# Performance work log

Hardware: AMD Instinct MI355X
Metric: run time of the kernel (lower is better)

The kernel has to match this reference:

```python
import jax, jax.numpy as jnp
import numpy as np

N_NODES = 100000
N_EDGES = 1600000
D_FEAT = 64
D_OUT = 64


def setup_inputs() -> dict:
    key = jax.random.key(0)
    ks = jax.random.split(key, 8)
    return {
        "feat": jax.random.normal(ks[0], (N_NODES, D_FEAT), dtype=jnp.float32),
        "emb": jax.random.normal(ks[1], (N_NODES, D_OUT), dtype=jnp.float32),
        "W1": jax.random.normal(ks[2], (D_OUT, D_FEAT), dtype=jnp.float32) * 0.1,
        "b1": jax.random.normal(ks[3], (D_OUT,), dtype=jnp.float32) * 0.1,
        "W2": jax.random.normal(ks[4], (D_OUT, D_OUT), dtype=jnp.float32) * 0.1,
        "b2": jax.random.normal(ks[5], (D_OUT,), dtype=jnp.float32) * 0.1,
        "edge_src": jax.random.randint(ks[6], (N_EDGES,), 0, N_NODES, dtype=jnp.int32),
        "edge_dst": jax.random.randint(ks[7], (N_EDGES,), 0, N_NODES, dtype=jnp.int32),
    }


def reference(feat, emb, W1, b1, W2, b2, edge_src, edge_dst):
    # n2v: per-node neighbor embedding sum (vectorized gather + segment-sum)
    n_nodes = feat.shape[0]
    nbr_sum = jax.ops.segment_sum(emb[edge_src], edge_dst, num_segments=n_nodes)  # [N, D_OUT]
    new_emb = jax.nn.relu(feat @ W1.T + b1 + nbr_sum @ W2.T + b2)  # [N, D_OUT]
    # g2v: graph embedding = sum of node embeddings
    graph_emb = new_emb.sum(axis=0)  # [D_OUT]
    return graph_emb
```

## Files before the change

### kernel.cpp

```cpp
#include <hip/hip_runtime.h>

#define N_NODES 100000
#define N_EDGES 1600000
#define D 64
#define CAP 32
#define OVF_CAP 8192
#define N_TILES 1563
#define NR 8
#define SLICE_EDGES 2048
#define N_SLICES 782
#define R1_BLOCKS 64
#define R1_ROWS 25
#define ASTRIDE 136

#define NB2 782
#define BCAP2 2560
#define EPB 8192
#define P1_BLOCKS 196
#define CVT_BLOCKS 128

typedef int    vint4  __attribute__((ext_vector_type(4)));
typedef short  s16x4  __attribute__((ext_vector_type(4)));
typedef short  s16x8  __attribute__((ext_vector_type(8)));
typedef float  f32x2  __attribute__((ext_vector_type(2)));
typedef float  f32x4  __attribute__((ext_vector_type(4)));
typedef __bf16 bf16x8 __attribute__((ext_vector_type(8)));

__device__ inline short f2bf(float f) {
    unsigned u = __builtin_bit_cast(unsigned, f);
    u += 0x7fffu + ((u >> 16) & 1u);
    return (short)(u >> 16);
}
__device__ inline s16x4 f2bf4(float4 v) {
    s16x4 r; r.x = f2bf(v.x); r.y = f2bf(v.y); r.z = f2bf(v.z); r.w = f2bf(v.w);
    return r;
}
__device__ inline float bf2f(short s) {
    return __builtin_bit_cast(float, ((unsigned)(unsigned short)s) << 16);
}

#define WS_SLOTS_OFF  401408
#define WS_ACC_OFF    13201408
#define WS_ACC16_OFF  13201408
#define WS_FEAT16_OFF 26001408
#define WS_OVFC_OFF   38801408
#define WS_OVF_OFF    38801424
#define WS_PART_OFF   38867200
#define WS_PART2_OFF  39267328
#define WS_EMB8_OFF   39283712
#define WS_W16_OFF    45683712
#define WS_NEEDED     (WS_PART2_OFF + R1_BLOCKS * 64 * 4)
#define WS_NEEDED16   (WS_W16_OFF + 64 * 128 * 2)

__global__ __launch_bounds__(512) void part_kernel(
    const int* __restrict__ edge_src, const int* __restrict__ edge_dst,
    int* __restrict__ bcnt, int* __restrict__ bkt,
    int* __restrict__ ovf_cnt, int2* __restrict__ ovf,
    const float* __restrict__ emb, unsigned* __restrict__ emb8,
    const float* __restrict__ feat, short* __restrict__ feat16,
    const float* __restrict__ W1, const float* __restrict__ W2,
    short* __restrict__ w16) {
    const int tid = threadIdx.x;
    if (blockIdx.x >= P1_BLOCKS) {
        const int rid = blockIdx.x - P1_BLOCKS;
        {
            const float4* e4 = (const float4*)emb;
            for (unsigned j = rid * 512 + tid; j < (unsigned)(N_NODES * D / 4);
                 j += CVT_BLOCKS * 512) {
                float4 v = e4[j];
                int w = 0;
                w = __builtin_amdgcn_cvt_pk_fp8_f32(v.x, v.y, w, false);
                w = __builtin_amdgcn_cvt_pk_fp8_f32(v.z, v.w, w, true);
                emb8[j] = (unsigned)w;
            }
        }
        {
            const float4* f4 = (const float4*)feat;
            for (unsigned k = rid * 512 + tid; k < (unsigned)(N_NODES * D / 8);
                 k += CVT_BLOCKS * 512) {
                float4 a = f4[k * 2];
                float4 b = f4[k * 2 + 1];
                s16x4 lo = f2bf4(a), hi = f2bf4(b);
                s16x8 pk = {lo.x, lo.y, lo.z, lo.w, hi.x, hi.y, hi.z, hi.w};
                *(s16x8*)&feat16[k * 8] = pk;
            }
        }
        if (rid == 0) {
            const float4* W1v = (const float4*)W1;
            const float4* W2v = (const float4*)W2;
            for (int k = tid; k < 64 * 16; k += 512) {
                const int row = k >> 4, c = k & 15;
                const float4 a = (c < 8) ? W1v[row * 16 + c * 2]
                                         : W2v[row * 16 + (c - 8) * 2];
                const float4 b = (c < 8) ? W1v[row * 16 + c * 2 + 1]
                                         : W2v[row * 16 + (c - 8) * 2 + 1];
                s16x4 lo = f2bf4(a), hi = f2bf4(b);
                s16x8 pk = {lo.x, lo.y, lo.z, lo.w, hi.x, hi.y, hi.z, hi.w};
                *(s16x8*)&w16[row * 128 + c * 8] = pk;
            }
        }
        return;
    }

    __shared__ int stage[EPB];
    __shared__ unsigned short bid[EPB];
    __shared__ int scA[1024];
    __shared__ int scB[1024];
    __shared__ int hist[NB2];
    int* const cur   = scB;
    int* const gbase = scA;

    const int e0 = blockIdx.x * EPB;
    for (int i = tid; i < NB2; i += 512) hist[i] = 0;
    __syncthreads();

    int ss[16], dd[16];
#pragma unroll
    for (int i = 0; i < 16; ++i) {
        const int e = e0 + i * 512 + tid;
        if (e < N_EDGES) { ss[i] = edge_src[e]; dd[i] = edge_dst[e]; }
        else             { ss[i] = 0; dd[i] = -1; }
    }

#pragma unroll
    for (int i = 0; i < 16; ++i)
        if (dd[i] >= 0) atomicAdd(&hist[dd[i] >> 7], 1);
    __syncthreads();

    scA[tid]       = (tid < NB2) ? hist[tid] : 0;
    scA[tid + 512] = 0;
    if (tid + 512 < NB2) scA[tid + 512] = hist[tid + 512];
    __syncthreads();
    {
        int* sA = scA;
        int* sB = scB;
        for (int off = 1; off < 1024; off <<= 1) {
            const int i1 = tid + 512;
            const int v0 = sA[tid] + ((tid >= off) ? sA[tid - off] : 0);
            const int v1 = sA[i1] + sA[i1 - off];
            sB[tid] = v0; sB[i1] = v1;
            __syncthreads();
            int* t = sA; sA = sB; sB = t;
        }
    }
    const int tot = scA[NB2 - 1];
    for (int i = tid; i < NB2; i += 512) cur[i] = scA[i] - hist[i];
    __syncthreads();

#pragma unroll
    for (int i = 0; i < 16; ++i) {
        if (dd[i] >= 0) {
            const int b = dd[i] >> 7;
            const int pos = atomicAdd(&cur[b], 1);
            stage[pos] = (ss[i] << 7) | (dd[i] & 127);
            bid[pos] = (unsigned short)b;
        }
    }
    for (int i = tid; i < NB2; i += 512)
        gbase[i] = atomicAdd(&bcnt[i], hist[i]);
    __syncthreads();

    for (int j = tid; j < tot; j += 512) {
        const int pk = stage[j];
        const int b  = bid[j];
        const int gpos = gbase[b] + (j - (cur[b] - hist[b]));
        if (gpos < BCAP2) {
            bkt[b * BCAP2 + gpos] = pk;
        } else {
            int oj = atomicAdd(ovf_cnt, 1);
            if (oj < OVF_CAP) ovf[oj] = make_int2(pk >> 7, (b << 7) | (pk & 127));
        }
    }
}

__global__ __launch_bounds__(512) void fill2_kernel(
    const int* __restrict__ bcnt, const int* __restrict__ bkt,
    int* __restrict__ cnt, int* __restrict__ slots,
    int* __restrict__ ovf_cnt, int2* __restrict__ ovf) {
    __shared__ int lcnt[128];
    const int b = blockIdx.x;
    const int tid = threadIdx.x;
    if (tid < 128) lcnt[tid] = 0;
    __syncthreads();
    int n = bcnt[b];
    if (n > BCAP2) n = BCAP2;
    for (int i = tid; i < n; i += 512) {
        const int pk = bkt[b * BCAP2 + i];
        const int dl = pk & 127;
        const int pos = atomicAdd(&lcnt[dl], 1);
        const int v = (b << 7) | dl;
        if (pos < CAP) {
            slots[v * CAP + pos] = pk >> 7;
        } else {
            int j = atomicAdd(ovf_cnt, 1);
            if (j < OVF_CAP) ovf[j] = make_int2(pk >> 7, v);
        }
    }
    __syncthreads();
    if (tid < 128) {
        const int v = (b << 7) | tid;
        if (v < N_NODES) cnt[v] = lcnt[tid];
    }
}

__global__ __launch_bounds__(256) void gather8_kernel(
    const unsigned* __restrict__ emb8, const int* __restrict__ cnt,
    const int* __restrict__ slots, short* __restrict__ acc16) {
    const int lane = threadIdx.x & 63;
    const int wave = threadIdx.x >> 6;
    const int v = blockIdx.x * 4 + wave;
    const int q = lane >> 4;
    const int c = lane & 15;
    int deg = cnt[v];
    if (deg > CAP) deg = CAP;
    const int si = slots[v * CAP + (lane & (CAP - 1))];

    float4 sum = make_float4(0.f, 0.f, 0.f, 0.f);
    for (int e = 0; e < deg; e += 8) {
        const int i0 = e + q, i1 = e + 4 + q;
        const int s0 = __shfl(si, i0 & (CAP - 1));
        const int s1 = __shfl(si, i1 & (CAP - 1));
        unsigned x0 = 0u, x1 = 0u;
        if (i0 < deg) x0 = emb8[(unsigned)s0 * 16 + c];
        if (i1 < deg) x1 = emb8[(unsigned)s1 * 16 + c];
        const f32x2 a0 = __builtin_amdgcn_cvt_pk_f32_fp8((int)x0, false);
        const f32x2 a1 = __builtin_amdgcn_cvt_pk_f32_fp8((int)x0, true);
        const f32x2 b0 = __builtin_amdgcn_cvt_pk_f32_fp8((int)x1, false);
        const f32x2 b1 = __builtin_amdgcn_cvt_pk_f32_fp8((int)x1, true);
        sum.x += a0.x + b0.x;
        sum.y += a0.y + b0.y;
        sum.z += a1.x + b1.x;
        sum.w += a1.y + b1.y;
    }
#pragma unroll
    for (int off = 16; off < 64; off <<= 1) {
        sum.x += __shfl_xor(sum.x, off);
        sum.y += __shfl_xor(sum.y, off);
        sum.z += __shfl_xor(sum.z, off);
        sum.w += __shfl_xor(sum.w, off);
    }
    if (q == 0) {
        *(s16x4*)&acc16[v * D + c * 4] = f2bf4(sum);
    }
}

__global__ __launch_bounds__(64) void ovf2_kernel(
    const float* __restrict__ emb, const int* __restrict__ ovf_cnt,
    const int2* __restrict__ ovf, short* __restrict__ acc16) {
    int n = *ovf_cnt;
    if (n > OVF_CAP) n = OVF_CAP;
    const int l = threadIdx.x;
    for (int i = 0; i < n; ++i) {
        const int2 e = ovf[i];
        const float a = bf2f(acc16[e.y * D + l]) + emb[e.x * D + l];
        acc16[e.y * D + l] = f2bf(a);
    }
}

__global__ __launch_bounds__(256) void fill_kernel(
    const int* __restrict__ edge_src, const int* __restrict__ edge_dst,
    int* __restrict__ cnt, int* __restrict__ slots,
    int* __restrict__ ovf_cnt, int2* __restrict__ ovf) {
    const int r = blockIdx.x & (NR - 1);
    if (r == 7) return;
    const int slice = blockIdx.x >> 3;
    const int base_e = slice * SLICE_EDGES + threadIdx.x * 8;
    if (base_e >= N_EDGES) return;
    const vint4* s4 = (const vint4*)(edge_src + base_e);
    const vint4* d4 = (const vint4*)(edge_dst + base_e);
    vint4 a0 = __builtin_nontemporal_load(s4);
    vint4 a1 = __builtin_nontemporal_load(s4 + 1);
    vint4 b0 = __builtin_nontemporal_load(d4);
    vint4 b1 = __builtin_nontemporal_load(d4 + 1);
    int ss[8] = {a0.x, a0.y, a0.z, a0.w, a1.x, a1.y, a1.z, a1.w};
    int dd[8] = {b0.x, b0.y, b0.z, b0.w, b1.x, b1.y, b1.z, b1.w};
    int pos[8];
#pragma unroll
    for (int i = 0; i < 8; ++i) {
        pos[i] = ((dd[i] >> 14) == r) ? atomicAdd(&cnt[dd[i]], 1) : -1;
    }
#pragma unroll
    for (int i = 0; i < 8; ++i) {
        if (pos[i] >= 0 && pos[i] < CAP) slots[dd[i] * CAP + pos[i]] = ss[i];
    }
#pragma unroll
    for (int i = 0; i < 8; ++i) {
        if (pos[i] >= CAP) {
            int j = atomicAdd(ovf_cnt, 1);
            if (j < OVF_CAP) ovf[j] = make_int2(ss[i], dd[i]);
        }
    }
}

__global__ __launch_bounds__(256) void gather_kernel(
    const float* __restrict__ emb, const int* __restrict__ cnt,
    const int* __restrict__ slots, float* __restrict__ acc) {
    const int lane = threadIdx.x & 63;
    const int wave = threadIdx.x >> 6;
    const int v = blockIdx.x * 4 + wave;
    const int q  = lane >> 4;
    const int c4 = lane & 15;
    int deg = cnt[v];
    if (deg > CAP) deg = CAP;
    const int si = slots[v * CAP + (lane & (CAP - 1))];
    const float4* emb4 = (const float4*)emb;

    float4 sum = make_float4(0.f, 0.f, 0.f, 0.f);
    for (int e = 0; e < deg; e += 4) {
        const int idx = e + q;
        const int s = __shfl(si, idx & (CAP - 1));
        if (idx < deg) {
            float4 a = emb4[s * 16 + c4];
            sum.x += a.x; sum.y += a.y; sum.z += a.z; sum.w += a.w;
        }
    }
#pragma unroll
    for (int off = 16; off < 64; off <<= 1) {
        sum.x += __shfl_xor(sum.x, off);
        sum.y += __shfl_xor(sum.y, off);
        sum.z += __shfl_xor(sum.z, off);
        sum.w += __shfl_xor(sum.w, off);
    }
    if (q == 0) {
        ((float4*)acc)[v * 16 + c4] = sum;
    }
}

__global__ __launch_bounds__(256) void ovf_kernel(
    const float* __restrict__ emb, const int* __restrict__ ovf_cnt,
    const int2* __restrict__ ovf, float* __restrict__ acc) {
    int n = *ovf_cnt;
    if (n > OVF_CAP) n = OVF_CAP;
    const int lane = threadIdx.x & 63;
    const int wv = (blockIdx.x * 256 + threadIdx.x) >> 6;
    const int nwaves = (gridDim.x * 256) >> 6;
    for (int i = wv; i < n; i += nwaves) {
        int2 e = ovf[i];
        unsafeAtomicAdd(&acc[e.y * D + lane], emb[e.x * D + lane]);
    }
}

__global__ __launch_bounds__(256) void scatter_kernel(
    const float* __restrict__ emb,
    const int* __restrict__ edge_src, const int* __restrict__ edge_dst,
    float* __restrict__ acc) {
    int gid = blockIdx.x * 256 + threadIdx.x;
    int e = gid >> 6;
    int c = gid & 63;
    unsafeAtomicAdd(&acc[edge_dst[e] * D + c], emb[edge_src[e] * D + c]);
}

__global__ __launch_bounds__(256) void final16_kernel(
    const short* __restrict__ feat16, const short* __restrict__ acc16,
    const short* __restrict__ w16, const float* __restrict__ b1,
    const float* __restrict__ b2, float* __restrict__ partials) {
    __shared__ short A_s[64 * ASTRIDE];
    __shared__ short W_s[64 * ASTRIDE];
    __shared__ float red[4][64];

    const int tid  = threadIdx.x;
    const int lane = tid & 63;
    const int wave = tid >> 6;
    const int quad = lane >> 4;
    const int col  = lane & 15;
    const int node0 = blockIdx.x * 64;

    float bias[4];
#pragma unroll
    for (int nb = 0; nb < 4; ++nb) {
        const int o = nb * 16 + col;
        bias[nb] = b1[o] + b2[o];
    }

#pragma unroll
    for (int i = 0; i < 4; ++i) {
        const int flat = tid + i * 256;
        const int row = flat >> 4, c = flat & 15;
        *(s16x8*)&W_s[row * ASTRIDE + c * 8] = *(const s16x8*)&w16[flat * 8];
    }

#pragma unroll
    for (int i = 0; i < 4; ++i) {
        const int flat = tid + i * 256;
        const int row = flat >> 4, c = flat & 15;
        const int node = node0 + row;
        s16x8 pk = {0, 0, 0, 0, 0, 0, 0, 0};
        if (node < N_NODES) {
            pk = (c < 8) ? *(const s16x8*)&feat16[node * D + c * 8]
                         : *(const s16x8*)&acc16[node * D + (c - 8) * 8];
        }
        *(s16x8*)&A_s[row * ASTRIDE + c * 8] = pk;
    }
    __syncthreads();

    bf16x8 Bf[4][4];
#pragma unroll
    for (int nb = 0; nb < 4; ++nb)
#pragma unroll
        for (int ks = 0; ks < 4; ++ks)
            Bf[nb][ks] = __builtin_bit_cast(bf16x8,
                *(const s16x8*)&W_s[(nb * 16 + col) * ASTRIDE + ks * 32 + quad * 8]);

    f32x4 C[4];
#pragma unroll
    for (int nb = 0; nb < 4; ++nb) C[nb] = (f32x4){0.f, 0.f, 0.f, 0.f};
#pragma unroll
    for (int ks = 0; ks < 4; ++ks) {
        const bf16x8 Af = __builtin_bit_cast(bf16x8,
            *(const s16x8*)&A_s[(wave * 16 + col) * ASTRIDE + ks * 32 + quad * 8]);
#pragma unroll
        for (int nb = 0; nb < 4; ++nb)
            C[nb] = __builtin_amdgcn_mfma_f32_16x16x32_bf16(Af, Bf[nb][ks],
                                                            C[nb], 0, 0, 0);
    }

    float sums[4] = {0.f, 0.f, 0.f, 0.f};
#pragma unroll
    for (int nb = 0; nb < 4; ++nb) {
#pragma unroll
        for (int reg = 0; reg < 4; ++reg) {
            const int node = node0 + wave * 16 + quad * 4 + reg;
            float u = C[nb][reg] + bias[nb];
            u = (u > 0.f) ? u : 0.f;
            if (node < N_NODES) sums[nb] += u;
        }
        sums[nb] += __shfl_xor(sums[nb], 16);
        sums[nb] += __shfl_xor(sums[nb], 32);
        if (lane < 16) red[wave][nb * 16 + lane] = sums[nb];
    }
    __syncthreads();
    if (tid < 64) {
        partials[blockIdx.x * 64 + tid] =
            red[0][tid] + red[1][tid] + red[2][tid] + red[3][tid];
    }
}

__global__ __launch_bounds__(256) void final_kernel(
    const float* __restrict__ feat, const float* __restrict__ acc,
    const float* __restrict__ W1, const float* __restrict__ b1,
    const float* __restrict__ W2, const float* __restrict__ b2,
    float* __restrict__ partials) {
    __shared__ short A_s[64 * ASTRIDE];
    __shared__ short W_s[64 * ASTRIDE];
    __shared__ float red[4][64];

    const int tid  = threadIdx.x;
    const int lane = tid & 63;
    const int wave = tid >> 6;
    const int quad = lane >> 4;
    const int col  = lane & 15;
    const int node0 = blockIdx.x * 64;

    float bias[4];
#pragma unroll
    for (int nb = 0; nb < 4; ++nb) {
        const int o = nb * 16 + col;
        bias[nb] = b1[o] + b2[o];
    }

    {
        const float4* W1v = (const float4*)W1;
        const float4* W2v = (const float4*)W2;
#pragma unroll
        for (int i = 0; i < 4; ++i) {
            const int flat = tid + i * 256;
            const int row = flat >> 4, c4 = flat & 15;
            *(s16x4*)&W_s[row * ASTRIDE + c4 * 4]      = f2bf4(W1v[flat]);
            *(s16x4*)&W_s[row * ASTRIDE + 64 + c4 * 4] = f2bf4(W2v[flat]);
        }
    }

    {
        const float4* fv = (const float4*)feat;
        const float4* av = (const float4*)acc;
#pragma unroll
        for (int i = 0; i < 4; ++i) {
            const int flat = tid + i * 256;
            const int row = flat >> 4, c4 = flat & 15;
            const int node = node0 + row;
            float4 f = make_float4(0.f, 0.f, 0.f, 0.f);
            float4 n = make_float4(0.f, 0.f, 0.f, 0.f);
            if (node < N_NODES) {
                f = fv[(size_t)node * 16 + c4];
                n = av[(size_t)node * 16 + c4];
            }
            *(s16x4*)&A_s[row * ASTRIDE + c4 * 4]      = f2bf4(f);
            *(s16x4*)&A_s[row * ASTRIDE + 64 + c4 * 4] = f2bf4(n);
        }
    }
    __syncthreads();

    bf16x8 Bf[4][4];
#pragma unroll
    for (int nb = 0; nb < 4; ++nb)
#pragma unroll
        for (int ks = 0; ks < 4; ++ks)
            Bf[nb][ks] = __builtin_bit_cast(bf16x8,
                *(const s16x8*)&W_s[(nb * 16 + col) * ASTRIDE + ks * 32 + quad * 8]);

    f32x4 C[4];
#pragma unroll
    for (int nb = 0; nb < 4; ++nb) C[nb] = (f32x4){0.f, 0.f, 0.f, 0.f};
#pragma unroll
    for (int ks = 0; ks < 4; ++ks) {
        const bf16x8 Af = __builtin_bit_cast(bf16x8,
            *(const s16x8*)&A_s[(wave * 16 + col) * ASTRIDE + ks * 32 + quad * 8]);
#pragma unroll
        for (int nb = 0; nb < 4; ++nb)
            C[nb] = __builtin_amdgcn_mfma_f32_16x16x32_bf16(Af, Bf[nb][ks],
                                                            C[nb], 0, 0, 0);
    }

    float sums[4] = {0.f, 0.f, 0.f, 0.f};
#pragma unroll
    for (int nb = 0; nb < 4; ++nb) {
#pragma unroll
        for (int reg = 0; reg < 4; ++reg) {
            const int node = node0 + wave * 16 + quad * 4 + reg;
            float u = C[nb][reg] + bias[nb];
            u = (u > 0.f) ? u : 0.f;
            if (node < N_NODES) sums[nb] += u;
        }
        sums[nb] += __shfl_xor(sums[nb], 16);
        sums[nb] += __shfl_xor(sums[nb], 32);
        if (lane < 16) red[wave][nb * 16 + lane] = sums[nb];
    }
    __syncthreads();
    if (tid < 64) {
        partials[blockIdx.x * 64 + tid] =
            red[0][tid] + red[1][tid] + red[2][tid] + red[3][tid];
    }
}

__global__ __launch_bounds__(256) void reduce1_kernel(
    const float* __restrict__ partials, float* __restrict__ part2) {
    __shared__ float red[4][64];
    const int col = threadIdx.x & 63;
    const int seg = threadIdx.x >> 6;
    const int r0 = blockIdx.x * R1_ROWS;
    int r1 = r0 + R1_ROWS;
    if (r1 > N_TILES) r1 = N_TILES;
    float s = 0.f;
    for (int r = r0 + seg; r < r1; r += 4) s += partials[r * 64 + col];
    red[seg][col] = s;
    __syncthreads();
    if (seg == 0) {
        part2[blockIdx.x * 64 + col] =
            red[0][col] + red[1][col] + red[2][col] + red[3][col];
    }
}

__global__ __launch_bounds__(256) void reduce2_kernel(
    const float* __restrict__ part2, float* __restrict__ out) {
    __shared__ float red[4][64];
    const int col = threadIdx.x & 63;
    const int seg = threadIdx.x >> 6;
    float s = 0.f;
    for (int r = seg; r < R1_BLOCKS; r += 4) s += part2[r * 64 + col];
    red[seg][col] = s;
    __syncthreads();
    if (seg == 0) {
        out[col] = red[0][col] + red[1][col] + red[2][col] + red[3][col];
    }
}

extern "C" void kernel_launch(void* const* d_in, const int* in_sizes, int n_in,
                              void* d_out, int out_size, void* d_ws, size_t ws_size,
                              hipStream_t stream) {
    const float* feat = (const float*)d_in[0];
    const float* emb  = (const float*)d_in[1];
    const float* W1   = (const float*)d_in[2];
    const float* b1   = (const float*)d_in[3];
    const float* W2   = (const float*)d_in[4];
    const float* b2   = (const float*)d_in[5];
    const int* edge_src = (const int*)d_in[6];
    const int* edge_dst = (const int*)d_in[7];
    float* out = (float*)d_out;
    char* ws = (char*)d_ws;

    if (ws_size >= (size_t)WS_NEEDED16) {
        int*      cnt      = (int*)ws;
        int*      slots    = (int*)(ws + WS_SLOTS_OFF);
        short*    acc16    = (short*)(ws + WS_ACC16_OFF);
        int*      bkt      = (int*)(ws + WS_ACC16_OFF);
        short*    feat16   = (short*)(ws + WS_FEAT16_OFF);
        int*      ovf_cnt  = (int*)(ws + WS_OVFC_OFF);
        int2*     ovf      = (int2*)(ws + WS_OVF_OFF);
        float*    partials = (float*)(ws + WS_PART_OFF);
        int*      bcnt     = (int*)(ws + WS_PART_OFF);
        float*    part2    = (float*)(ws + WS_PART2_OFF);
        unsigned* emb8     = (unsigned*)(ws + WS_EMB8_OFF);
        short*    w16      = (short*)(ws + WS_W16_OFF);

        (void)hipMemsetAsync(ovf_cnt, 0, sizeof(int), stream);
        (void)hipMemsetAsync(bcnt, 0, NB2 * sizeof(int), stream);

        part_kernel<<<P1_BLOCKS + CVT_BLOCKS, 512, 0, stream>>>(
            edge_src, edge_dst, bcnt, bkt, ovf_cnt, ovf,
            emb, emb8, feat, feat16, W1, W2, w16);
        fill2_kernel<<<NB2, 512, 0, stream>>>(bcnt, bkt, cnt, slots,
                                              ovf_cnt, ovf);
        gather8_kernel<<<N_NODES / 4, 256, 0, stream>>>(emb8, cnt, slots, acc16);
        ovf2_kernel<<<1, 64, 0, stream>>>(emb, ovf_cnt, ovf, acc16);

        final16_kernel<<<N_TILES, 256, 0, stream>>>(feat16, acc16, w16,
                                                    b1, b2, partials);
        reduce1_kernel<<<R1_BLOCKS, 256, 0, stream>>>(partials, part2);
        reduce2_kernel<<<1, 256, 0, stream>>>(part2, out);
    } else if (ws_size >= (size_t)WS_NEEDED) {
        int*   cnt      = (int*)ws;
        int*   slots    = (int*)(ws + WS_SLOTS_OFF);
        float* acc      = (float*)(ws + WS_ACC_OFF);
        int*   ovf_cnt  = (int*)(ws + WS_OVFC_OFF);
        int2*  ovf      = (int2*)(ws + WS_OVF_OFF);
        float* partials = (float*)(ws + WS_PART_OFF);
        float* part2    = (float*)(ws + WS_PART2_OFF);

        (void)hipMemsetAsync(cnt, 0, N_NODES * sizeof(int), stream);
        (void)hipMemsetAsync(ovf_cnt, 0, sizeof(int), stream);

        fill_kernel<<<NR * N_SLICES, 256, 0, stream>>>(edge_src, edge_dst,
                                                       cnt, slots, ovf_cnt, ovf);
        gather_kernel<<<N_NODES / 4, 256, 0, stream>>>(emb, cnt, slots, acc);
        ovf_kernel<<<16, 256, 0, stream>>>(emb, ovf_cnt, ovf, acc);

        final_kernel<<<N_TILES, 256, 0, stream>>>(feat, acc, W1, b1, W2, b2,
                                                  partials);
        reduce1_kernel<<<R1_BLOCKS, 256, 0, stream>>>(partials, part2);
        reduce2_kernel<<<1, 256, 0, stream>>>(part2, out);
    } else {
        float* acc = (float*)ws;
        (void)hipMemsetAsync(acc, 0, (size_t)N_NODES * D * sizeof(float), stream);
        scatter_kernel<<<(N_EDGES * 64) / 256, 256, 0, stream>>>(emb, edge_src,
                                                                 edge_dst, acc);
        float* partials = (float*)(ws + (size_t)N_NODES * D * sizeof(float));
        float* part2    = partials + (size_t)N_TILES * 64;
        final_kernel<<<N_TILES, 256, 0, stream>>>(feat, acc, W1, b1, W2, b2,
                                                  partials);
        reduce1_kernel<<<R1_BLOCKS, 256, 0, stream>>>(partials, part2);
        reduce2_kernel<<<1, 256, 0, stream>>>(part2, out);
    }
}
```

Measured before the change: 197.6 us.

## Fuse feat/W bf16 conversion into final GEMM kernel and unroll gather loop

Drops the separate feat-to-bf16 and W-to-bf16 conversion passes from the partition kernel. The final kernel now reads fp32 feat and W1/W2 directly and converts them to bf16 while staging into shared memory, which avoids writing and re-reading a feat16 copy. It also halves the number of conversion blocks and fully unrolls the gather loop to CAP with predicated loads. The cost is that every tile converts W redundantly, and the unrolled gather issues shuffles for empty slots on low-degree nodes.

```diff
diff --git a/kernel.cpp b/kernel.cpp
--- a/kernel.cpp
+++ b/kernel.cpp
@@ -17,7 +17,7 @@
 #define BCAP2 2560
 #define EPB 8192
 #define P1_BLOCKS 196
-#define CVT_BLOCKS 128
+#define CVT_BLOCKS 64
 
 typedef int    vint4  __attribute__((ext_vector_type(4)));
 typedef short  s16x4  __attribute__((ext_vector_type(4)));
@@ -42,62 +42,30 @@
 #define WS_SLOTS_OFF  401408
 #define WS_ACC_OFF    13201408
 #define WS_ACC16_OFF  13201408
-#define WS_FEAT16_OFF 26001408
 #define WS_OVFC_OFF   38801408
 #define WS_OVF_OFF    38801424
 #define WS_PART_OFF   38867200
 #define WS_PART2_OFF  39267328
 #define WS_EMB8_OFF   39283712
-#define WS_W16_OFF    45683712
 #define WS_NEEDED     (WS_PART2_OFF + R1_BLOCKS * 64 * 4)
-#define WS_NEEDED16   (WS_W16_OFF + 64 * 128 * 2)
+#define WS_NEEDED16   (WS_EMB8_OFF + N_NODES * D * 2)
 
 __global__ __launch_bounds__(512) void part_kernel(
     const int* __restrict__ edge_src, const int* __restrict__ edge_dst,
     int* __restrict__ bcnt, int* __restrict__ bkt,
     int* __restrict__ ovf_cnt, int2* __restrict__ ovf,
-    const float* __restrict__ emb, unsigned* __restrict__ emb8,
-    const float* __restrict__ feat, short* __restrict__ feat16,
-    const float* __restrict__ W1, const float* __restrict__ W2,
-    short* __restrict__ w16) {
+    const float* __restrict__ emb, unsigned* __restrict__ emb8) {
     const int tid = threadIdx.x;
     if (blockIdx.x >= P1_BLOCKS) {
-        const int rid = blockIdx.x - P1_BLOCKS;
-        {
-            const float4* e4 = (const float4*)emb;
-            for (unsigned j = rid * 512 + tid; j < (unsigned)(N_NODES * D / 4);
-                 j += CVT_BLOCKS * 512) {
-                float4 v = e4[j];
-                int w = 0;
-                w = __builtin_amdgcn_cvt_pk_fp8_f32(v.x, v.y, w, false);
-                w = __builtin_amdgcn_cvt_pk_fp8_f32(v.z, v.w, w, true);
-                emb8[j] = (unsigned)w;
-            }
-        }
-        {
-            const float4* f4 = (const float4*)feat;
-            for (unsigned k = rid * 512 + tid; k < (unsigned)(N_NODES * D / 8);
-                 k += CVT_BLOCKS * 512) {
-                float4 a = f4[k * 2];
-                float4 b = f4[k * 2 + 1];
-                s16x4 lo = f2bf4(a), hi = f2bf4(b);
-                s16x8 pk = {lo.x, lo.y, lo.z, lo.w, hi.x, hi.y, hi.z, hi.w};
-                *(s16x8*)&feat16[k * 8] = pk;
-            }
-        }
-        if (rid == 0) {
-            const float4* W1v = (const float4*)W1;
-            const float4* W2v = (const float4*)W2;
-            for (int k = tid; k < 64 * 16; k += 512) {
-                const int row = k >> 4, c = k & 15;
-                const float4 a = (c < 8) ? W1v[row * 16 + c * 2]
-                                         : W2v[row * 16 + (c - 8) * 2];
-                const float4 b = (c < 8) ? W1v[row * 16 + c * 2 + 1]
-                                         : W2v[row * 16 + (c - 8) * 2 + 1];
-                s16x4 lo = f2bf4(a), hi = f2bf4(b);
-                s16x8 pk = {lo.x, lo.y, lo.z, lo.w, hi.x, hi.y, hi.z, hi.w};
-                *(s16x8*)&w16[row * 128 + c * 8] = pk;
-            }
+        const float4* e4 = (const float4*)emb;
+        const unsigned t0 = (blockIdx.x - P1_BLOCKS) * 512 + tid;
+        for (unsigned j = t0; j < (unsigned)(N_NODES * D / 4);
+             j += CVT_BLOCKS * 512) {
+            float4 v = e4[j];
+            int w = 0;
+            w = __builtin_amdgcn_cvt_pk_fp8_f32(v.x, v.y, w, false);
+            w = __builtin_amdgcn_cvt_pk_fp8_f32(v.z, v.w, w, true);
+            emb8[j] = (unsigned)w;
         }
         return;
     }
@@ -216,10 +184,11 @@
     const int si = slots[v * CAP + (lane & (CAP - 1))];
 
     float4 sum = make_float4(0.f, 0.f, 0.f, 0.f);
-    for (int e = 0; e < deg; e += 8) {
+#pragma unroll
+    for (int e = 0; e < CAP; e += 8) {
         const int i0 = e + q, i1 = e + 4 + q;
-        const int s0 = __shfl(si, i0 & (CAP - 1));
-        const int s1 = __shfl(si, i1 & (CAP - 1));
+        const int s0 = __shfl(si, i0);
+        const int s1 = __shfl(si, i1);
         unsigned x0 = 0u, x1 = 0u;
         if (i0 < deg) x0 = emb8[(unsigned)s0 * 16 + c];
         if (i1 < deg) x1 = emb8[(unsigned)s1 * 16 + c];
@@ -350,10 +319,11 @@
     unsafeAtomicAdd(&acc[edge_dst[e] * D + c], emb[edge_src[e] * D + c]);
 }
 
-__global__ __launch_bounds__(256) void final16_kernel(
-    const short* __restrict__ feat16, const short* __restrict__ acc16,
-    const short* __restrict__ w16, const float* __restrict__ b1,
-    const float* __restrict__ b2, float* __restrict__ partials) {
+__global__ __launch_bounds__(256) void final_mixed_kernel(
+    const float* __restrict__ feat, const short* __restrict__ acc16,
+    const float* __restrict__ W1, const float* __restrict__ b1,
+    const float* __restrict__ W2, const float* __restrict__ b2,
+    float* __restrict__ partials) {
     __shared__ short A_s[64 * ASTRIDE];
     __shared__ short W_s[64 * ASTRIDE];
     __shared__ float red[4][64];
@@ -372,24 +342,40 @@
         bias[nb] = b1[o] + b2[o];
     }
 
-#pragma unroll
-    for (int i = 0; i < 4; ++i) {
-        const int flat = tid + i * 256;
-        const int row = flat >> 4, c = flat & 15;
-        *(s16x8*)&W_s[row * ASTRIDE + c * 8] = *(const s16x8*)&w16[flat * 8];
-    }
-
-#pragma unroll
-    for (int i = 0; i < 4; ++i) {
-        const int flat = tid + i * 256;
-        const int row = flat >> 4, c = flat & 15;
-        const int node = node0 + row;
-        s16x8 pk = {0, 0, 0, 0, 0, 0, 0, 0};
-        if (node < N_NODES) {
-            pk = (c < 8) ? *(const s16x8*)&feat16[node * D + c * 8]
-                         : *(const s16x8*)&acc16[node * D + (c - 8) * 8];
-        }
-        *(s16x8*)&A_s[row * ASTRIDE + c * 8] = pk;
+    {
+        const float4* W1v = (const float4*)W1;
+        const float4* W2v = (const float4*)W2;
+#pragma unroll
+        for (int i = 0; i < 4; ++i) {
+            const int flat = tid + i * 256;
+            const int row = flat >> 4, c4 = flat & 15;
+            *(s16x4*)&W_s[row * ASTRIDE + c4 * 4]      = f2bf4(W1v[flat]);
+            *(s16x4*)&W_s[row * ASTRIDE + 64 + c4 * 4] = f2bf4(W2v[flat]);
+        }
+    }
+
+    {
+        const float4* fv = (const float4*)feat;
+#pragma unroll
+        for (int i = 0; i < 4; ++i) {
+            const int flat = tid + i * 256;
+            const int row = flat >> 4, c4 = flat & 15;
+            const int node = node0 + row;
+            float4 f = make_float4(0.f, 0.f, 0.f, 0.f);
+            if (node < N_NODES) f = fv[(size_t)node * 16 + c4];
+            *(s16x4*)&A_s[row * ASTRIDE + c4 * 4] = f2bf4(f);
+        }
+    }
+    {
+#pragma unroll
+        for (int i = 0; i < 2; ++i) {
+            const int flat = tid + i * 256;
+            const int row = flat >> 3, c = flat & 7;
+            const int node = node0 + row;
+            s16x8 pk = {0, 0, 0, 0, 0, 0, 0, 0};
+            if (node < N_NODES) pk = *(const s16x8*)&acc16[node * D + c * 8];
+            *(s16x8*)&A_s[row * ASTRIDE + 64 + c * 8] = pk;
+        }
     }
     __syncthreads();
 
@@ -583,28 +569,25 @@
         int*      slots    = (int*)(ws + WS_SLOTS_OFF);
         short*    acc16    = (short*)(ws + WS_ACC16_OFF);
         int*      bkt      = (int*)(ws + WS_ACC16_OFF);
-        short*    feat16   = (short*)(ws + WS_FEAT16_OFF);
         int*      ovf_cnt  = (int*)(ws + WS_OVFC_OFF);
         int2*     ovf      = (int2*)(ws + WS_OVF_OFF);
         float*    partials = (float*)(ws + WS_PART_OFF);
         int*      bcnt     = (int*)(ws + WS_PART_OFF);
         float*    part2    = (float*)(ws + WS_PART2_OFF);
         unsigned* emb8     = (unsigned*)(ws + WS_EMB8_OFF);
-        short*    w16      = (short*)(ws + WS_W16_OFF);
 
         (void)hipMemsetAsync(ovf_cnt, 0, sizeof(int), stream);
         (void)hipMemsetAsync(bcnt, 0, NB2 * sizeof(int), stream);
 
         part_kernel<<<P1_BLOCKS + CVT_BLOCKS, 512, 0, stream>>>(
-            edge_src, edge_dst, bcnt, bkt, ovf_cnt, ovf,
-            emb, emb8, feat, feat16, W1, W2, w16);
+            edge_src, edge_dst, bcnt, bkt, ovf_cnt, ovf, emb, emb8);
         fill2_kernel<<<NB2, 512, 0, stream>>>(bcnt, bkt, cnt, slots,
                                               ovf_cnt, ovf);
         gather8_kernel<<<N_NODES / 4, 256, 0, stream>>>(emb8, cnt, slots, acc16);
         ovf2_kernel<<<1, 64, 0, stream>>>(emb, ovf_cnt, ovf, acc16);
 
-        final16_kernel<<<N_TILES, 256, 0, stream>>>(feat16, acc16, w16,
-                                                    b1, b2, partials);
+        final_mixed_kernel<<<N_TILES, 256, 0, stream>>>(feat, acc16, W1, b1,
+                                                        W2, b2, partials);
         reduce1_kernel<<<R1_BLOCKS, 256, 0, stream>>>(partials, part2);
         reduce2_kernel<<<1, 256, 0, stream>>>(part2, out);
     } else if (ws_size >= (size_t)WS_NEEDED) {
```

After: 191.7 us. 3.0% less time.
